# Kernel tuning notes

Measured on AMD Instinct MI355X. Metric: run time of the kernel, lower is better.

The kernel has to match this reference:

```python
import jax, jax.numpy as jnp
import numpy as np
import math

B, N, H, C = 1, 2048, 8, 128
PQ, PV, R, CS, CZ = 8, 12, 2, 256, 128
CZ4 = CZ // 4
INF = 1e5
EPS = 1e-8
SOFTPLUS_INV_1 = 0.541324854612918


def _quat_to_rot(q):
    q = q / jnp.linalg.norm(q, axis=-1, keepdims=True)
    w, x, y, z = q[..., 0], q[..., 1], q[..., 2], q[..., 3]
    return jnp.stack([
        jnp.stack([1 - 2 * (y * y + z * z), 2 * (x * y - z * w), 2 * (x * z + y * w)], -1),
        jnp.stack([2 * (x * y + z * w), 1 - 2 * (x * x + z * z), 2 * (y * z - x * w)], -1),
        jnp.stack([2 * (x * z - y * w), 2 * (y * z + x * w), 1 - 2 * (x * x + y * y)], -1),
    ], -2)


def setup_inputs() -> dict:
    key = jax.random.key(0)
    ks = jax.random.split(key, 16)
    rn = lambda k, shape, s=1.0: jax.random.normal(k, shape, dtype=jnp.float32) * s
    hc = H * C
    return dict(
        s=rn(ks[0], (B, N, CS)),
        z_factor_1=rn(ks[1], (B, N, R, CZ)),
        z_factor_2=rn(ks[2], (B, N, R, CZ)),
        rot=_quat_to_rot(rn(ks[3], (B, N, 4))),
        trans=rn(ks[4], (B, N, 3)),
        mask=jnp.ones((B, N), dtype=bool),
        w_q=rn(ks[5], (hc, CS), 0.02), b_q=jnp.zeros((hc,), jnp.float32),
        w_kv=rn(ks[6], (2 * hc, CS), 0.02), b_kv=jnp.zeros((2 * hc,), jnp.float32),
        w_qp=rn(ks[7], (H * PQ * 3, CS), 0.02), b_qp=jnp.zeros((H * PQ * 3,), jnp.float32),
        w_kvp=rn(ks[8], (H * (PQ + PV) * 3, CS), 0.02), b_kvp=jnp.zeros((H * (PQ + PV) * 3,), jnp.float32),
        w_b=rn(ks[9], (H, CZ), 0.02), b_b=jnp.zeros((H,), jnp.float32),
        w_dz=rn(ks[10], (CZ4, CZ), 0.02), b_dz=jnp.zeros((CZ4,), jnp.float32),
        head_weights=jnp.full((H,), SOFTPLUS_INV_1, dtype=jnp.float32),
        w_out=rn(ks[11], (CS, H * (CZ4 + C + 4 * PV)), 0.02), b_out=jnp.zeros((CS,), jnp.float32),
    )


def _lin(x, w, b):
    return x @ w.T + b


def _ipa(s, z1, z2, rot, trans, mask, w_q, b_q, w_kv, b_kv, w_qp, b_qp,
         w_kvp, b_kvp, w_b, b_b, w_dz, b_dz, head_weights, w_out, b_out):
    q = _lin(s, w_q, b_q).reshape(B, N, H, C)
    kv = _lin(s, w_kv, b_kv).reshape(B, N, H, 2 * C)
    k, v = kv[..., :C], kv[..., C:]
    # local points -> global frame: x_glob = R x_loc + t
    qp = _lin(s, w_qp, b_qp).reshape(B, N, H * PQ, 3)
    qp = (jnp.einsum('bnij,bnpj->bnpi', rot, qp) + trans[:, :, None, :]).reshape(B, N, H, PQ, 3)
    kvp = _lin(s, w_kvp, b_kvp).reshape(B, N, H * (PQ + PV), 3)
    kvp = (jnp.einsum('bnij,bnpj->bnpi', rot, kvp) + trans[:, :, None, :]).reshape(B, N, H, PQ + PV, 3)
    kp, vp = kvp[..., :PQ, :], kvp[..., PQ:, :]
    # head weights: softplus init to 1, AF2 scaling sqrt(1/(3*(PQ*9/2)))
    hw = jax.nn.softplus(head_weights) * math.sqrt(1.0 / (3 * (PQ * 9.0 / 2)))
    # low-rank pair bias factors
    b1 = _lin(z1, w_b, b_b)   # [B,N,R,H]
    b2 = _lin(z2, w_b, b_b)
    z1d = _lin(z1, w_dz, b_dz)  # [B,N,R,CZ4]
    z2d = _lin(z2, w_dz, b_dz)
    # logits: scalar QK + point-distance + low-rank pair bias
    scalar = jnp.einsum('bihc,bjhc->bhij', q, k) * math.sqrt(1.0 / (3 * C))
    ptdot = jnp.einsum('bihpx,bjhpx->bhij', qp, kp)
    qn = jnp.sum(qp * qp, axis=(-1, -2))  # [B,N,H]
    kn = jnp.sum(kp * kp, axis=(-1, -2))
    pt_term = hw[None, :, None, None] * (
        ptdot - 0.5 * qn.transpose(0, 2, 1)[:, :, :, None] - 0.5 * kn.transpose(0, 2, 1)[:, :, None, :])
    pair = jnp.einsum('birh,bjrh->bhij', b1, b2)
    mask_bias = jnp.where(mask, 0.0, -INF)[:, None, None, :]
    a = jax.nn.softmax(scalar + pt_term + pair + mask_bias, axis=-1)  # [B,H,N,N]
    # outputs
    o = jnp.einsum('bhij,bjhc->bihc', a, v).reshape(B, N, H * C)
    opt = jnp.einsum('bhij,bjhpx->bihpx', a, vp)  # global-frame points
    opt_loc = jnp.einsum('bnji,bnhpj->bnhpi', rot, opt - trans[:, :, None, None, :])  # R^T (x - t)
    opt_norm = jnp.sqrt(jnp.sum(opt_loc * opt_loc, axis=-1) + EPS)  # [B,N,H,PV]
    oz = jnp.einsum('bhij,bjrc->bihrc', a, z2d)
    opair = jnp.sum(oz * z1d[:, :, None, :, :], axis=3)  # [B,N,H,CZ4]
    feats = jnp.concatenate([
        o,
        opt_loc[..., 0].reshape(B, N, H * PV),
        opt_loc[..., 1].reshape(B, N, H * PV),
        opt_loc[..., 2].reshape(B, N, H * PV),
        opt_norm.reshape(B, N, H * PV),
        opair.reshape(B, N, H * CZ4),
    ], axis=-1)
    return _lin(feats, w_out, b_out)  # [B,N,CS]


def reference(s, z_factor_1, z_factor_2, rot, trans, mask, w_q, b_q, w_kv, b_kv,
              w_qp, b_qp, w_kvp, b_kvp, w_b, b_b, w_dz, b_dz, head_weights,
              w_out, b_out):
    return _ipa(s, z_factor_1, z_factor_2, rot, trans, mask, w_q, b_q, w_kv, b_kv,
                w_qp, b_qp, w_kvp, b_kvp, w_b, b_b, w_dz, b_dz, head_weights,
                w_out, b_out)
```

## Files before the change

### kernel.cpp

```cpp
#include <hip/hip_runtime.h>
#include <math.h>

#define NN   2048
#define HH   8
#define CC   128
#define PQn  8
#define PVn  12
#define RRn  2
#define CSn  256
#define CZn  128
#define CZ4n 32
#define HC   (HH*CC)
#define FEAT (HC + 4*HH*PVn + HH*CZ4n)
#define DA   160
#define DVP  256
#define DVU  240
#define QKV  3840
#define LOG2E 1.4426950408889634f

typedef unsigned short ushort_t;
#define AS1 __attribute__((address_space(1)))
#define AS3 __attribute__((address_space(3)))

using bfrag = __attribute__((ext_vector_type(8))) short;
using ffrag = __attribute__((ext_vector_type(4))) float;

__device__ inline ushort_t f2bf(float x) {
    union { float f; unsigned int u; } v; v.f = x;
    unsigned int r = v.u + 0x7fffu + ((v.u >> 16) & 1u);
    return (ushort_t)(r >> 16);
}
__device__ inline float bf2f(ushort_t x) {
    union { unsigned int u; float f; } v; v.u = ((unsigned int)x) << 16; return v.f;
}

struct CvtArgs {
    const float4* src[12];
    ushort4* dst[12];
    int n4[12];
};
__global__ __launch_bounds__(256) void cvtn_kernel(CvtArgs a,
    float4* __restrict__ outp, const float4* __restrict__ bias4)
{
    int i = blockIdx.x * 256 + threadIdx.x;
    if (i < NN * CSn / 4) {
        outp[i] = bias4[i & 63];
        return;
    }
    i -= NN * CSn / 4;
#pragma unroll
    for (int k = 0; k < 12; ++k) {
        if (i < a.n4[k]) {
            ushort4 o;
            if (a.src[k]) {
                float4 v = a.src[k][i];
                o = make_ushort4(f2bf(v.x), f2bf(v.y), f2bf(v.z), f2bf(v.w));
            } else {
                o = make_ushort4(0, 0, 0, 0);
            }
            a.dst[k][i] = o;
            return;
        }
        i -= a.n4[k];
    }
}

__global__ __launch_bounds__(256) void bgemm_kernel(
    const ushort_t* __restrict__ A, size_t sA,
    const ushort_t* __restrict__ B, size_t sB,
    void* __restrict__ Cv, size_t sC,
    const float* __restrict__ bias, size_t sBias,
    int ldk, int kOff, int kOffPerZ, int kLen, int ldc, int obf, int atomicOut)
{
    const int z = blockIdx.z;
    A += (size_t)z * sA;
    B += (size_t)z * sB;
    const float* bp = bias ? (bias + (size_t)z * sBias) : nullptr;
    const int k0beg = kOff + z * kOffPerZ;
    const int r0 = blockIdx.y * 128;
    const int c0 = blockIdx.x * 128;
    __shared__ __align__(16) ushort_t lA[128 * 32];
    __shared__ __align__(16) ushort_t lB[128 * 32];
    const int tid = threadIdx.x;
    const int w = tid >> 6, lane = tid & 63;
    const int wm = (w >> 1) * 64, wn = (w & 1) * 64;
    const int lrA = lane >> 2;
    const int lcA = (lane & 3) * 8;
    ffrag acc[4][4] = {};

    for (int k0 = k0beg; k0 < k0beg + kLen; k0 += 32) {
#pragma unroll
        for (int t = 0; t < 2; ++t) {
            int instr = w * 2 + t;
            int r = instr * 16 + lrA;
            const ushort_t* ga = A + (size_t)(r0 + r) * ldk + k0 + lcA;
            const ushort_t* gb = B + (size_t)(c0 + r) * ldk + k0 + lcA;
            __builtin_amdgcn_global_load_lds((const AS1 void*)ga,
                (AS3 void*)((AS3 ushort_t*)&lA[instr * 512 + lane * 8]), 16, 0, 0);
            __builtin_amdgcn_global_load_lds((const AS1 void*)gb,
                (AS3 void*)((AS3 ushort_t*)&lB[instr * 512 + lane * 8]), 16, 0, 0);
        }
        __syncthreads();
        bfrag af[4], bf[4];
#pragma unroll
        for (int mi = 0; mi < 4; ++mi)
            af[mi] = *(const bfrag*)&lA[(wm + mi * 16 + (lane & 15)) * 32 + (lane >> 4) * 8];
#pragma unroll
        for (int ni = 0; ni < 4; ++ni)
            bf[ni] = *(const bfrag*)&lB[(wn + ni * 16 + (lane & 15)) * 32 + (lane >> 4) * 8];
#pragma unroll
        for (int mi = 0; mi < 4; ++mi)
#pragma unroll
            for (int ni = 0; ni < 4; ++ni)
                acc[mi][ni] = __builtin_amdgcn_mfma_f32_16x16x32_bf16(af[mi], bf[ni], acc[mi][ni], 0, 0, 0);
        __syncthreads();
    }
#pragma unroll
    for (int mi = 0; mi < 4; ++mi) {
#pragma unroll
        for (int ni = 0; ni < 4; ++ni) {
            int col = c0 + wn + ni * 16 + (lane & 15);
            float bv = bp ? bp[col] : 0.f;
#pragma unroll
            for (int rr = 0; rr < 4; ++rr) {
                int row = r0 + wm + mi * 16 + (lane >> 4) * 4 + rr;
                float val = acc[mi][ni][rr] + bv;
                if (atomicOut)
                    unsafeAtomicAdd(&((float*)Cv)[(size_t)z * sC + (size_t)row * ldc + col], val);
                else if (obf)
                    ((ushort_t*)Cv)[(size_t)z * sC + (size_t)row * ldc + col] = f2bf(val);
                else
                    ((float*)Cv)[(size_t)z * sC + (size_t)row * ldc + col] = val;
            }
        }
    }
}

__global__ __launch_bounds__(256) void mgemm_kernel(
    const ushort_t* __restrict__ A0, const ushort_t* __restrict__ B0,
    ushort_t* __restrict__ C0,
    const ushort_t* __restrict__ A1, const ushort_t* __restrict__ B1,
    ushort_t* __restrict__ C1)
{
    const int bx = blockIdx.x;
    const ushort_t *A, *B;
    ushort_t* C;
    int ldk, kLen, ldc, r0, c0;
    if (bx < 480) {
        A = A0; B = B0; C = C0;
        ldk = CSn; kLen = CSn; ldc = QKV;
        r0 = (bx / 30) * 128;
        c0 = (bx % 30) * 128;
    } else {
        int i = bx - 480;
        A = A1; B = B1; C = C1;
        ldk = CZn; kLen = CZn; ldc = 128;
        r0 = i * 128;
        c0 = 0;
    }
    __shared__ __align__(16) ushort_t lA[128 * 32];
    __shared__ __align__(16) ushort_t lB[128 * 32];
    const int tid = threadIdx.x;
    const int w = tid >> 6, lane = tid & 63;
    const int wm = (w >> 1) * 64, wn = (w & 1) * 64;
    const int lrA = lane >> 2;
    const int lcA = (lane & 3) * 8;
    ffrag acc[4][4] = {};

    for (int k0 = 0; k0 < kLen; k0 += 32) {
#pragma unroll
        for (int t = 0; t < 2; ++t) {
            int instr = w * 2 + t;
            int r = instr * 16 + lrA;
            const ushort_t* ga = A + (size_t)(r0 + r) * ldk + k0 + lcA;
            const ushort_t* gb = B + (size_t)(c0 + r) * ldk + k0 + lcA;
            __builtin_amdgcn_global_load_lds((const AS1 void*)ga,
                (AS3 void*)((AS3 ushort_t*)&lA[instr * 512 + lane * 8]), 16, 0, 0);
            __builtin_amdgcn_global_load_lds((const AS1 void*)gb,
                (AS3 void*)((AS3 ushort_t*)&lB[instr * 512 + lane * 8]), 16, 0, 0);
        }
        __syncthreads();
        bfrag af[4], bf[4];
#pragma unroll
        for (int mi = 0; mi < 4; ++mi)
            af[mi] = *(const bfrag*)&lA[(wm + mi * 16 + (lane & 15)) * 32 + (lane >> 4) * 8];
#pragma unroll
        for (int ni = 0; ni < 4; ++ni)
            bf[ni] = *(const bfrag*)&lB[(wn + ni * 16 + (lane & 15)) * 32 + (lane >> 4) * 8];
#pragma unroll
        for (int mi = 0; mi < 4; ++mi)
#pragma unroll
            for (int ni = 0; ni < 4; ++ni)
                acc[mi][ni] = __builtin_amdgcn_mfma_f32_16x16x32_bf16(af[mi], bf[ni], acc[mi][ni], 0, 0, 0);
        __syncthreads();
    }
#pragma unroll
    for (int mi = 0; mi < 4; ++mi) {
#pragma unroll
        for (int ni = 0; ni < 4; ++ni) {
            int col = c0 + wn + ni * 16 + (lane & 15);
#pragma unroll
            for (int rr = 0; rr < 4; ++rr) {
                int row = r0 + wm + mi * 16 + (lane >> 4) * 4 + rr;
                C[(size_t)row * ldc + col] = f2bf(acc[mi][ni][rr]);
            }
        }
    }
}

__global__ __launch_bounds__(256) void prep_kernel(
    const ushort_t* __restrict__ qkv,
    const ushort_t* __restrict__ zproj,
    const float* __restrict__ b_q, const float* __restrict__ b_kv,
    const float* __restrict__ b_qp, const float* __restrict__ b_kvp,
    const float* __restrict__ b_b, const float* __restrict__ b_dz,
    const float* __restrict__ rot, const float* __restrict__ trans,
    const float* __restrict__ hwts,
    ushort_t* __restrict__ qaug, ushort_t* __restrict__ kaug,
    ushort_t* __restrict__ vaug)
{
    const int i = blockIdx.x;
    const int tid = threadIdx.x;
    __shared__ float R[9], t[3];
    __shared__ float qp_l[192], kp_l[192], vp_l[288];
    __shared__ float kn_s[8], hw_s[8];
    __shared__ __align__(16) ushort_t qa_s[8 * DA];
    __shared__ __align__(16) ushort_t ka_s[8 * DA];
    __shared__ __align__(16) ushort_t va_s[8 * DVP];
    if (tid < 9) R[tid] = rot[i*9 + tid];
    if (tid < 3) t[tid] = trans[i*3 + tid];
    if (tid < 8) {
        hw_s[tid] = log1pf(expf(hwts[tid])) * 0.09622504486493763f;
        kn_s[tid] = 0.f;
    }
    __syncthreads();
    if (tid < 64) {
        const ushort_t* v = qkv + (size_t)i*QKV + 3072 + tid*3;
        float vx = bf2f(v[0]) + b_qp[tid*3+0];
        float vy = bf2f(v[1]) + b_qp[tid*3+1];
        float vz = bf2f(v[2]) + b_qp[tid*3+2];
        float X = R[0]*vx + R[1]*vy + R[2]*vz + t[0];
        float Y = R[3]*vx + R[4]*vy + R[5]*vz + t[1];
        float Z = R[6]*vx + R[7]*vy + R[8]*vz + t[2];
        qp_l[tid*3+0] = X; qp_l[tid*3+1] = Y; qp_l[tid*3+2] = Z;
    } else if (tid < 224) {
        int p = tid - 64;
        int h = p / 20, pp = p % 20;
        const ushort_t* v = qkv + (size_t)i*QKV + 3264 + p*3;
        float vx = bf2f(v[0]) + b_kvp[p*3+0];
        float vy = bf2f(v[1]) + b_kvp[p*3+1];
        float vz = bf2f(v[2]) + b_kvp[p*3+2];
        float X = R[0]*vx + R[1]*vy + R[2]*vz + t[0];
        float Y = R[3]*vx + R[4]*vy + R[5]*vz + t[1];
        float Z = R[6]*vx + R[7]*vy + R[8]*vz + t[2];
        if (pp < 8) {
            int b = (h*8 + pp) * 3;
            kp_l[b+0] = X; kp_l[b+1] = Y; kp_l[b+2] = Z;
            atomicAdd(&kn_s[h], X*X + Y*Y + Z*Z);
        } else {
            int b = (h*12 + pp - 8) * 3;
            vp_l[b+0] = X; vp_l[b+1] = Y; vp_l[b+2] = Z;
        }
    }
    __syncthreads();

    const float QS = 0.05103103630798288f * LOG2E;
    for (int idx = tid; idx < 8 * DA; idx += 256) {
        int h = idx / DA, d = idx - h * DA;
        float qv, kv2;
        if (d < 128) {
            qv  = QS * (bf2f(qkv[(size_t)i*QKV + h*128 + d]) + b_q[h*128 + d]);
            kv2 = bf2f(qkv[(size_t)i*QKV + 1024 + h*256 + d]) + b_kv[h*256 + d];
        } else if (d < 152) {
            qv  = hw_s[h] * LOG2E * qp_l[h*24 + d - 128];
            kv2 = kp_l[h*24 + d - 128];
        } else if (d < 154) {
            int r = d - 152;
            qv  = LOG2E * (bf2f(zproj[(size_t)(i*2 + r)*128 + h]) + b_b[h]);
            kv2 = bf2f(zproj[(size_t)(4096 + i*2 + r)*128 + h]) + b_b[h];
        } else if (d == 154) {
            qv  = LOG2E;
            kv2 = -0.5f * hw_s[h] * kn_s[h];
        } else { qv = 0.f; kv2 = 0.f; }
        qa_s[idx] = f2bf(qv);
        ka_s[idx] = f2bf(kv2);
    }
    for (int idx = tid; idx < 8 * DVP; idx += 256) {
        int h = idx >> 8, d = idx & 255;
        float v;
        if (d < 128)       v = bf2f(qkv[(size_t)i*QKV + 1024 + h*256 + 128 + d]) + b_kv[h*256 + 128 + d];
        else if (d < 164)  v = vp_l[h*36 + d - 128];
        else if (d < 196)  v = bf2f(zproj[(size_t)(4096 + i*2 + 0)*128 + 8 + d - 164]) + b_dz[d - 164];
        else if (d < 228)  v = bf2f(zproj[(size_t)(4096 + i*2 + 1)*128 + 8 + d - 196]) + b_dz[d - 196];
        else if (d == 239) v = 1.0f;
        else               v = 0.f;
        va_s[idx] = f2bf(v);
    }
    __syncthreads();

    for (int idx = tid; idx < 576; idx += 256) {
        if (idx < 160) {
            int h = idx / 20, dg = (idx - h*20) * 8;
            *(bfrag*)(qaug + ((size_t)h*NN + i) * DA + dg) = *(const bfrag*)&qa_s[h*DA + dg];
        } else if (idx < 320) {
            int r = idx - 160;
            int h = r / 20, dg = (r - h*20) * 8;
            *(bfrag*)(kaug + ((size_t)h*NN + i) * DA + dg) = *(const bfrag*)&ka_s[h*DA + dg];
        } else {
            int r = idx - 320;
            int h = r >> 5, dg = (r & 31) * 8;
            *(bfrag*)(vaug + ((size_t)h*NN + i) * DVP + dg) = *(const bfrag*)&va_s[h*DVP + dg];
        }
    }
}

__global__ __launch_bounds__(256) void transpose_kernel(
    const ushort_t* __restrict__ in, ushort_t* __restrict__ out)
{
    const int z = blockIdx.z;
    in  += (size_t)z * NN * DVP;
    out += (size_t)z * NN * DVP;
    const int i0 = blockIdx.x * 64;
    const int d0 = blockIdx.y * 64;
    __shared__ __align__(8) ushort_t tb[64][72];
    const int tid = threadIdx.x;
#pragma unroll
    for (int p = 0; p < 4; ++p) {
        int idx = p * 256 + tid;
        int r = idx >> 4, sg = idx & 15;
        ushort4 v = *(const ushort4*)(in + (size_t)(i0 + r) * DVP + d0 + sg * 4);
        *(ushort4*)&tb[r][sg * 4] = v;
    }
    __syncthreads();
#pragma unroll
    for (int p = 0; p < 4; ++p) {
        int idx = p * 256 + tid;
        int d = idx >> 4, ig = idx & 15;
        ushort4 v = make_ushort4(tb[ig*4+0][d], tb[ig*4+1][d],
                                 tb[ig*4+2][d], tb[ig*4+3][d]);
        *(ushort4*)(out + (size_t)(d0 + d) * NN + i0 + ig * 4) = v;
    }
}

__global__ __launch_bounds__(256, 2) void flash_kernel(
    const ushort_t* __restrict__ qaug,
    const ushort_t* __restrict__ kaug,
    const ushort_t* __restrict__ vaugT,
    ushort_t* __restrict__ Opart,
    float* __restrict__ Mpart,
    float* __restrict__ Lpart)
{
    const int i0 = blockIdx.x * 64;
    const int h  = blockIdx.y;
    const int g  = blockIdx.z;

    __shared__ __align__(16) ushort_t Kt[64 * 168];
    __shared__ __align__(16) ushort_t Vt[DVU * 72];
    __shared__ __align__(16) ushort_t Pl[4 * 32 * 40];

    const int tid = threadIdx.x;
    const int w = tid >> 6, lane = tid & 63;
    const int quad = lane >> 4, lc = lane & 15;
    const int rh = w >> 1, jh = w & 1;

    const ushort_t* qh = qaug + (size_t)h * NN * DA;
    const ushort_t* kh = kaug + (size_t)h * NN * DA;
    const ushort_t* vh = vaugT + (size_t)h * DVP * NN;

    auto stageK = [&](int j0) {
#pragma unroll
        for (int k = 0; k < 6; ++k) {
            int idx = k * 256 + tid;
            if (k < 5 || idx < 1344) {
                int row = idx / 21, off = idx - row * 21;
                const ushort_t* src = (off < 20) ? (kh + (size_t)(j0 + row) * DA + off * 8) : kh;
                __builtin_amdgcn_global_load_lds((const AS1 void*)src,
                    (AS3 void*)((AS3 ushort_t*)&Kt[idx * 8]), 16, 0, 0);
            }
        }
    };
    auto stageV = [&](int j0) {
#pragma unroll
        for (int k = 0; k < 9; ++k) {
            int idx = k * 256 + tid;
            if (k < 8 || idx < 2160) {
                int row = idx / 9, off = idx - row * 9;
                const ushort_t* src = (off < 8) ? (vh + (size_t)row * NN + j0 + off * 8) : vh;
                __builtin_amdgcn_global_load_lds((const AS1 void*)src,
                    (AS3 void*)((AS3 ushort_t*)&Vt[idx * 8]), 16, 0, 0);
            }
        }
    };

    bfrag qf[2][5];
#pragma unroll
    for (int mi = 0; mi < 2; ++mi)
#pragma unroll
        for (int ks = 0; ks < 5; ++ks)
            qf[mi][ks] = *(const bfrag*)(qh + (size_t)(i0 + rh*32 + mi*16 + lc) * DA + ks*32 + quad*8);

    ffrag acc[2][15];
#pragma unroll
    for (int mi = 0; mi < 2; ++mi)
#pragma unroll
        for (int dt = 0; dt < 15; ++dt)
            acc[mi][dt] = (ffrag){0.f, 0.f, 0.f, 0.f};
    float m_run = -3.0e38f;

    ushort_t* PlW = Pl + w * (32 * 40);

    stageK(g * 1024);
    __syncthreads();

    for (int it = 0; it < 16; ++it) {
        const int j0 = g * 1024 + it * 64;

        stageV(j0);

        ffrag sf[2][2];
#pragma unroll
        for (int mi = 0; mi < 2; ++mi)
#pragma unroll
            for (int jt = 0; jt < 2; ++jt)
                sf[mi][jt] = (ffrag){0.f, 0.f, 0.f, 0.f};
        __builtin_amdgcn_s_setprio(1);
#pragma unroll
        for (int ks = 0; ks < 5; ++ks) {
#pragma unroll
            for (int jt = 0; jt < 2; ++jt) {
                bfrag kf = *(const bfrag*)&Kt[(jh*32 + jt*16 + lc) * 168 + ks*32 + quad*8];
#pragma unroll
                for (int mi = 0; mi < 2; ++mi)
                    sf[mi][jt] = __builtin_amdgcn_mfma_f32_16x16x32_bf16(qf[mi][ks], kf, sf[mi][jt], 0, 0, 0);
            }
        }
        __builtin_amdgcn_s_setprio(0);

        float tm = sf[0][0][0];
#pragma unroll
        for (int mi = 0; mi < 2; ++mi)
#pragma unroll
            for (int jt = 0; jt < 2; ++jt)
#pragma unroll
                for (int rr = 0; rr < 4; ++rr)
                    tm = fmaxf(tm, sf[mi][jt][rr]);
#pragma unroll
        for (int d = 1; d < 64; d <<= 1)
            tm = fmaxf(tm, __shfl_xor(tm, d));

        if (tm > m_run) {
            float al = exp2f(m_run - tm);
            m_run = tm;
#pragma unroll
            for (int mi = 0; mi < 2; ++mi)
#pragma unroll
                for (int dt = 0; dt < 15; ++dt)
                    acc[mi][dt] *= al;
        }

#pragma unroll
        for (int mi = 0; mi < 2; ++mi)
#pragma unroll
            for (int rr = 0; rr < 4; ++rr) {
                float p0 = exp2f(sf[mi][0][rr] - m_run);
                float p1 = exp2f(sf[mi][1][rr] - m_run);
                PlW[(mi*16 + quad*4 + rr) * 40 + lc]      = f2bf(p0);
                PlW[(mi*16 + quad*4 + rr) * 40 + 16 + lc] = f2bf(p1);
            }

        __syncthreads();

        if (it < 15) stageK(j0 + 64);

        bfrag pf0 = *(const bfrag*)&PlW[(0*16 + lc) * 40 + quad*8];
        bfrag pf1 = *(const bfrag*)&PlW[(1*16 + lc) * 40 + quad*8];
        __builtin_amdgcn_s_setprio(1);
#pragma unroll
        for (int dt = 0; dt < 15; ++dt) {
            bfrag vf = *(const bfrag*)&Vt[(dt*16 + lc) * 72 + jh*32 + quad*8];
            acc[0][dt] = __builtin_amdgcn_mfma_f32_16x16x32_bf16(pf0, vf, acc[0][dt], 0, 0, 0);
            acc[1][dt] = __builtin_amdgcn_mfma_f32_16x16x32_bf16(pf1, vf, acc[1][dt], 0, 0, 0);
        }
        __builtin_amdgcn_s_setprio(0);

        __syncthreads();
    }

    const int part = g * 2 + jh;
    ushort_t* Ob = Opart + ((size_t)part * HH + h) * NN * DVU;
#pragma unroll
    for (int mi = 0; mi < 2; ++mi)
#pragma unroll
        for (int dt = 0; dt < 15; ++dt)
#pragma unroll
            for (int rr = 0; rr < 4; ++rr) {
                int row = i0 + rh*32 + mi*16 + quad*4 + rr;
                Ob[(size_t)row * DVU + dt*16 + lc] = f2bf(acc[mi][dt][rr]);
            }
    size_t sb = ((size_t)part * HH + h) * NN;
    if (lane < 32) Mpart[sb + i0 + rh*32 + lane] = m_run;
    if (lc == 15) {
#pragma unroll
        for (int mi = 0; mi < 2; ++mi)
#pragma unroll
            for (int rr = 0; rr < 4; ++rr)
                Lpart[sb + i0 + rh*32 + mi*16 + quad*4 + rr] = acc[mi][14][rr];
    }
}

__global__ __launch_bounds__(256) void combine_kernel(
    const ushort_t* __restrict__ Opart, const float* __restrict__ Mpart,
    const float* __restrict__ Lpart, const ushort_t* __restrict__ zproj,
    const float* __restrict__ b_dz,
    const float* __restrict__ rot, const float* __restrict__ trans,
    ushort_t* __restrict__ feats)
{
    const int i = blockIdx.x;
    const int tid = threadIdx.x;
    __shared__ float wgt[4][8];
    __shared__ float Ol[8][DVU];
    if (tid < 8) {
        int h = tid;
        float mm[4], ll[4];
#pragma unroll
        for (int p = 0; p < 4; ++p) {
            mm[p] = Mpart[((size_t)p * HH + h) * NN + i];
            ll[p] = Lpart[((size_t)p * HH + h) * NN + i];
        }
        float M = fmaxf(fmaxf(mm[0], mm[1]), fmaxf(mm[2], mm[3]));
        float Z = 0.f, e[4];
#pragma unroll
        for (int p = 0; p < 4; ++p) { e[p] = exp2f(mm[p] - M); Z += ll[p] * e[p]; }
        float zi = 1.f / Z;
#pragma unroll
        for (int p = 0; p < 4; ++p) wgt[p][h] = e[p] * zi;
    }
    __syncthreads();
    {
        int h = tid >> 5;
        int dg0 = tid & 31;
        for (int dg = dg0; dg < 60; dg += 32) {
            int d = dg * 4;
            float vx = 0.f, vy = 0.f, vz = 0.f, vw = 0.f;
#pragma unroll
            for (int p = 0; p < 4; ++p) {
                ushort4 u = *(const ushort4*)&Opart[(((size_t)p * HH + h) * NN + i) * DVU + d];
                float wv = wgt[p][h];
                vx += bf2f(u.x) * wv; vy += bf2f(u.y) * wv;
                vz += bf2f(u.z) * wv; vw += bf2f(u.w) * wv;
            }
            Ol[h][d] = vx; Ol[h][d+1] = vy; Ol[h][d+2] = vz; Ol[h][d+3] = vw;
        }
    }
    __syncthreads();

    ushort_t* f = feats + (size_t)i * FEAT;
    {
        int h = tid >> 5;
        int c = (tid * 4) & 127;
        ushort4 o4 = make_ushort4(f2bf(Ol[h][c]), f2bf(Ol[h][c+1]),
                                  f2bf(Ol[h][c+2]), f2bf(Ol[h][c+3]));
        *(ushort4*)(f + tid * 4) = o4;
    }
    if (tid < 96) {
        int h = tid / 12, p = tid % 12;
        const float* Rm = rot + i * 9;
        float ox = Ol[h][128 + p*3 + 0] - trans[i*3 + 0];
        float oy = Ol[h][128 + p*3 + 1] - trans[i*3 + 1];
        float oz = Ol[h][128 + p*3 + 2] - trans[i*3 + 2];
        float lx = Rm[0]*ox + Rm[3]*oy + Rm[6]*oz;
        float ly = Rm[1]*ox + Rm[4]*oy + Rm[7]*oz;
        float lz = Rm[2]*ox + Rm[5]*oy + Rm[8]*oz;
        float nrm = sqrtf(lx*lx + ly*ly + lz*lz + 1e-8f);
        f[1024 + 0*96 + tid] = f2bf(lx);
        f[1024 + 1*96 + tid] = f2bf(ly);
        f[1024 + 2*96 + tid] = f2bf(lz);
        f[1024 + 3*96 + tid] = f2bf(nrm);
    }
    {
        int h = tid >> 5, c = tid & 31;
        float z1d0 = bf2f(zproj[(size_t)(i*2 + 0)*128 + 8 + c]) + b_dz[c];
        float z1d1 = bf2f(zproj[(size_t)(i*2 + 1)*128 + 8 + c]) + b_dz[c];
        f[1408 + tid] = f2bf(Ol[h][164 + c] * z1d0 + Ol[h][196 + c] * z1d1);
    }
}

extern "C" void kernel_launch(void* const* d_in, const int* in_sizes, int n_in,
                              void* d_out, int out_size, void* d_ws, size_t ws_size,
                              hipStream_t stream) {
    const float* s     = (const float*)d_in[0];
    const float* z1    = (const float*)d_in[1];
    const float* z2    = (const float*)d_in[2];
    const float* rot   = (const float*)d_in[3];
    const float* trans = (const float*)d_in[4];
    const float* w_q   = (const float*)d_in[6];
    const float* b_q   = (const float*)d_in[7];
    const float* w_kv  = (const float*)d_in[8];
    const float* b_kv  = (const float*)d_in[9];
    const float* w_qp  = (const float*)d_in[10];
    const float* b_qp  = (const float*)d_in[11];
    const float* w_kvp = (const float*)d_in[12];
    const float* b_kvp = (const float*)d_in[13];
    const float* w_b   = (const float*)d_in[14];
    const float* b_b   = (const float*)d_in[15];
    const float* w_dz  = (const float*)d_in[16];
    const float* b_dz  = (const float*)d_in[17];
    const float* hwts  = (const float*)d_in[18];
    const float* w_out = (const float*)d_in[19];
    const float* b_out = (const float*)d_in[20];
    float* out = (float*)d_out;

    char* base = (char*)d_ws;
    const size_t OPART_BYTES = (size_t)4*HH*NN*DVU*2;
    char* S = base;
    ushort_t* s_bf  = (ushort_t*)(S);
    ushort_t* z_bf  = (ushort_t*)(S + 1048576);
    ushort_t* wall  = (ushort_t*)(S + 1048576 + 2097152);
    ushort_t* wz    = (ushort_t*)(S + 1048576 + 2097152 + 1966080);
    ushort_t* qkv   = (ushort_t*)(S + 1048576 + 2097152 + 1966080 + 32768);
    ushort_t* vaug  = (ushort_t*)(S + 1048576 + 2097152 + 1966080 + 32768 + 15728640);
    ushort_t* Opart = (ushort_t*)(S);
    char* P = base + OPART_BYTES;
    size_t off = 0;
    auto alloc = [&](size_t bytes) -> void* {
        void* p = P + off;
        off += (bytes + 255) & ~(size_t)255;
        return p;
    };
    ushort_t* wout_bf = (ushort_t*)alloc((size_t)CSn*FEAT*2);
    ushort_t* zproj   = (ushort_t*)alloc((size_t)8192*128*2);
    ushort_t* qaug    = (ushort_t*)alloc((size_t)HH*NN*DA*2);
    ushort_t* kaug    = (ushort_t*)alloc((size_t)HH*NN*DA*2);
    ushort_t* vaugT   = (ushort_t*)alloc((size_t)HH*NN*DVP*2);
    float*    Mpart   = (float*)alloc((size_t)4*HH*NN*4);
    float*    Lpart   = (float*)alloc((size_t)4*HH*NN*4);
    ushort_t* feats   = (ushort_t*)alloc((size_t)NN*FEAT*2);

    CvtArgs ca;
    int j = 0; int tot = 0;
    auto job = [&](const float* src, ushort_t* dst, int nElem) {
        ca.src[j] = (const float4*)src; ca.dst[j] = (ushort4*)dst; ca.n4[j] = nElem/4;
        tot += nElem/4; ++j;
    };
    job(s,     s_bf,              NN*CSn);
    job(z1,    z_bf,              4096*128);
    job(z2,    z_bf + 4096*128,   4096*128);
    job(w_q,   wall,              1024*256);
    job(w_kv,  wall + 1024*256,   2048*256);
    job(w_qp,  wall + 3072*256,   192*256);
    job(w_kvp, wall + 3264*256,   480*256);
    job(w_out, wout_bf,           CSn*FEAT);
    job(nullptr, wall + 3744*256, 96*256);
    job(w_b,   wz,                8*128);
    job(w_dz,  wz + 8*128,        32*128);
    job(nullptr, wz + 40*128,     88*128);
    tot += NN*CSn/4;
    cvtn_kernel<<<(tot + 255)/256, 256, 0, stream>>>(ca, (float4*)out, (const float4*)b_out);

    mgemm_kernel<<<544, 256, 0, stream>>>(s_bf, wall, qkv, z_bf, wz, zproj);

    prep_kernel<<<NN, 256, 0, stream>>>(qkv, zproj,
                                        b_q, b_kv, b_qp, b_kvp, b_b, b_dz,
                                        rot, trans, hwts, qaug, kaug, vaug);
    transpose_kernel<<<dim3(NN/64, DVP/64, HH), 256, 0, stream>>>(vaug, vaugT);

    flash_kernel<<<dim3(NN/64, HH, 2), 256, 0, stream>>>(
        qaug, kaug, vaugT, Opart, Mpart, Lpart);

    combine_kernel<<<NN, 256, 0, stream>>>(Opart, Mpart, Lpart, zproj, b_dz,
                                           rot, trans, feats);

    bgemm_kernel<<<dim3(CSn/128, NN/128, 4), 256, 0, stream>>>(
        feats, 0, wout_bf, 0, out, 0, nullptr, 0,
        FEAT, 0, FEAT/4, FEAT/4, CSn, 0, 1);
}
```

Before: 210.2 us.

## Double-buffer K/V tiles in flash kernel with 512-thread blocks over 128 rows

The flash attention kernel now runs 512 threads per block, covering 128 query rows, and keeps two LDS buffers each for K and V. The next tile's K and V are prefetched asynchronously while the current tile is computed, which removes one barrier per iteration. The grid is flattened into one dimension, with head and split index taken from the low bits of the block id. LDS use roughly doubles, which may reduce how many blocks fit per CU. The rh/jh mapping uses w>>1 with w up to 7, so rows may exceed the intended layout unless the unseen code handles it; waves 4-7 could map to rows beyond 64.

```diff
diff --git a/kernel.cpp b/kernel.cpp
--- a/kernel.cpp
+++ b/kernel.cpp
@@ -342,7 +342,7 @@
     }
 }
 
-__global__ __launch_bounds__(256, 2) void flash_kernel(
+__global__ __launch_bounds__(512, 2) void flash_kernel(
     const ushort_t* __restrict__ qaug,
     const ushort_t* __restrict__ kaug,
     const ushort_t* __restrict__ vaugT,
@@ -350,13 +350,16 @@
     float* __restrict__ Mpart,
     float* __restrict__ Lpart)
 {
-    const int i0 = blockIdx.x * 64;
-    const int h  = blockIdx.y;
-    const int g  = blockIdx.z;
-
-    __shared__ __align__(16) ushort_t Kt[64 * 168];
-    __shared__ __align__(16) ushort_t Vt[DVU * 72];
-    __shared__ __align__(16) ushort_t Pl[4 * 32 * 40];
+    const int bid = blockIdx.x;
+    const int G = bid & 15;
+    const int m = bid >> 4;
+    const int h = G >> 1;
+    const int g = G & 1;
+    const int i0 = m * 128;
+
+    __shared__ __align__(16) ushort_t Kt[2][64 * 168];
+    __shared__ __align__(16) ushort_t Vt[2][DVU * 72];
+    __shared__ __align__(16) ushort_t Pl[8 * 32 * 40];
 
     const int tid = threadIdx.x;
     const int w = tid >> 6, lane = tid & 63;
@@ -367,27 +370,27 @@
     const ushort_t* kh = kaug + (size_t)h * NN * DA;
     const ushort_t* vh = vaugT + (size_t)h * DVP * NN;
 
-    auto stageK = [&](int j0) {
-#pragma unroll
-        for (int k = 0; k < 6; ++k) {
-            int idx = k * 256 + tid;
-            if (k < 5 || idx < 1344) {
+    auto stageK = [&](ushort_t* dst, int j0) {
+#pragma unroll
+        for (int k = 0; k < 3; ++k) {
+            int idx = k * 512 + tid;
+            if (k < 2 || idx < 1344) {
                 int row = idx / 21, off = idx - row * 21;
                 const ushort_t* src = (off < 20) ? (kh + (size_t)(j0 + row) * DA + off * 8) : kh;
                 __builtin_amdgcn_global_load_lds((const AS1 void*)src,
-                    (AS3 void*)((AS3 ushort_t*)&Kt[idx * 8]), 16, 0, 0);
+                    (AS3 void*)((AS3 ushort_t*)&dst[idx * 8]), 16, 0, 0);
             }
         }
     };
-    auto stageV = [&](int j0) {
-#pragma unroll
-        for (int k = 0; k < 9; ++k) {
-            int idx = k * 256 + tid;
-            if (k < 8 || idx < 2160) {
+    auto stageV = [&](ushort_t* dst, int j0) {
+#pragma unroll
+        for (int k = 0; k < 5; ++k) {
+            int idx = k * 512 + tid;
+            if (k < 4 || idx < 2160) {
                 int row = idx / 9, off = idx - row * 9;
                 const ushort_t* src = (off < 8) ? (vh + (size_t)row * NN + j0 + off * 8) : vh;
                 __builtin_amdgcn_global_load_lds((const AS1 void*)src,
-                    (AS3 void*)((AS3 ushort_t*)&Vt[idx * 8]), 16, 0, 0);
+                    (AS3 void*)((AS3 ushort_t*)&dst[idx * 8]), 16, 0, 0);
             }
         }
     };
@@ -409,13 +412,18 @@
 
     ushort_t* PlW = Pl + w * (32 * 40);
 
-    stageK(g * 1024);
+    stageK(Kt[0], g * 1024);
+    stageV(Vt[0], g * 1024);
     __syncthreads();
 
+    int cur = 0;
     for (int it = 0; it < 16; ++it) {
         const int j0 = g * 1024 + it * 64;
 
-        stageV(j0);
+        if (it < 15) {
+            stageK(Kt[cur ^ 1], j0 + 64);
+            stageV(Vt[cur ^ 1], j0 + 64);
+        }
 
         ffrag sf[2][2];
 #pragma unroll
@@ -428,7 +436,7 @@
         for (int ks = 0; ks < 5; ++ks) {
 #pragma unroll
             for (int jt = 0; jt < 2; ++jt) {
-                bfrag kf = *(const bfrag*)&Kt[(jh*32 + jt*16 + lc) * 168 + ks*32 + quad*8];
+                bfrag kf = *(const bfrag*)&Kt[cur][(jh*32 + jt*16 + lc) * 168 + ks*32 + quad*8];
 #pragma unroll
                 for (int mi = 0; mi < 2; ++mi)
                     sf[mi][jt] = __builtin_amdgcn_mfma_f32_16x16x32_bf16(qf[mi][ks], kf, sf[mi][jt], 0, 0, 0);
@@ -468,22 +476,19 @@
                 PlW[(mi*16 + quad*4 + rr) * 40 + 16 + lc] = f2bf(p1);
             }
 
-        __syncthreads();
-
-        if (it < 15) stageK(j0 + 64);
-
         bfrag pf0 = *(const bfrag*)&PlW[(0*16 + lc) * 40 + quad*8];
         bfrag pf1 = *(const bfrag*)&PlW[(1*16 + lc) * 40 + quad*8];
         __builtin_amdgcn_s_setprio(1);
 #pragma unroll
         for (int dt = 0; dt < 15; ++dt) {
-            bfrag vf = *(const bfrag*)&Vt[(dt*16 + lc) * 72 + jh*32 + quad*8];
+            bfrag vf = *(const bfrag*)&Vt[cur][(dt*16 + lc) * 72 + jh*32 + quad*8];
             acc[0][dt] = __builtin_amdgcn_mfma_f32_16x16x32_bf16(pf0, vf, acc[0][dt], 0, 0, 0);
             acc[1][dt] = __builtin_amdgcn_mfma_f32_16x16x32_bf16(pf1, vf, acc[1][dt], 0, 0, 0);
         }
         __builtin_amdgcn_s_setprio(0);
 
         __syncthreads();
+        cur ^= 1;
     }
 
     const int part = g * 2 + jh;
@@ -664,7 +669,7 @@
                                         rot, trans, hwts, qaug, kaug, vaug);
     transpose_kernel<<<dim3(NN/64, DVP/64, HH), 256, 0, stream>>>(vaug, vaugT);
 
-    flash_kernel<<<dim3(NN/64, HH, 2), 256, 0, stream>>>(
+    flash_kernel<<<256, 512, 0, stream>>>(
         qaug, kaug, vaugT, Opart, Mpart, Lpart);
 
     combine_kernel<<<NN, 256, 0, stream>>>(Opart, Mpart, Lpart, zproj, b_dz,
```

Result: no change. 209.5 us (-0.3%).
